# Optimization experiments

Measured on AMD Instinct MI355X. Metric: run time of the kernel, lower is better.

## Reference

```python
import jax, jax.numpy as jnp
import numpy as np

N, L, I, H, D = 8192, 8, 256, 512, 8
PER = N // D  # nodes per depth level; level 0 nodes are tree roots


def setup_inputs() -> dict:
    key = jax.random.key(0)
    ks = jax.random.split(key, 9)
    s = 0.05
    x_seq = jax.random.normal(ks[0], (N, L, I), jnp.float32)
    # GRU params (torch nn.GRU layout, gate order r,z,n), stored transposed [in, 3H]
    W_ih = jax.random.normal(ks[1], (I, 3 * H), jnp.float32) * s
    W_hh = jax.random.normal(ks[2], (H, 3 * H), jnp.float32) * s
    b_ih = jax.random.normal(ks[3], (3 * H,), jnp.float32) * s
    b_hh = jax.random.normal(ks[4], (3 * H,), jnp.float32) * s
    # Child-sum TreeLSTM params: x-projections for i,o,u,f and recurrent U's
    Wx = jax.random.normal(ks[5], (H, 4 * H), jnp.float32) * s
    bx = jax.random.normal(ks[6], (4 * H,), jnp.float32) * s
    U_iou = jax.random.normal(ks[7], (H, 3 * H), jnp.float32) * s
    U_f = jax.random.normal(ks[8], (H, H), jnp.float32) * s
    # Forest structure: D levels of PER nodes; node at level d>0 has a random
    # parent at level d-1; roots (level 0) point at themselves (contribution is
    # zero because their own state is still zero when level 0 is processed).
    rng = np.random.default_rng(0)
    depth = np.repeat(np.arange(D), PER).astype(np.int32)
    parent = np.arange(N, dtype=np.int32)
    for d in range(1, D):
        parent[d * PER:(d + 1) * PER] = rng.integers((d - 1) * PER, d * PER, PER)
    root_ids = np.arange(PER, dtype=np.int32)
    return {
        "x_seq": x_seq, "W_ih": W_ih, "W_hh": W_hh, "b_ih": b_ih, "b_hh": b_hh,
        "Wx": Wx, "bx": bx, "U_iou": U_iou, "U_f": U_f,
        "parent": jnp.asarray(parent), "depth": jnp.asarray(depth),
        "root_ids": jnp.asarray(root_ids), "n_levels": D,
    }


def reference(x_seq, W_ih, W_hh, b_ih, b_hh, Wx, bx, U_iou, U_f,
              parent, depth, root_ids, n_levels):
    n = x_seq.shape[0]
    h_dim = W_hh.shape[0]

    # --- GRU over each node's encoding sequence (all nodes batched) ---
    def gru_step(h, x_t):  # h: [N,H], x_t: [N,I]
        gi = x_t @ W_ih + b_ih
        gh = h @ W_hh + b_hh
        ir, iz, inn = jnp.split(gi, 3, axis=-1)
        hr, hz, hn = jnp.split(gh, 3, axis=-1)
        r = jax.nn.sigmoid(ir + hr)
        z = jax.nn.sigmoid(iz + hz)
        ng = jnp.tanh(inn + r * hn)
        return (1.0 - z) * ng + z * h, None

    h0 = jnp.zeros((n, h_dim), x_seq.dtype)
    enc, _ = jax.lax.scan(gru_step, h0, jnp.swapaxes(x_seq, 0, 1))  # [N,H]

    # --- Child-sum TreeLSTM, processed leaves -> roots by depth level ---
    xg = enc @ Wx + bx  # [N,4H]
    xi, xo, xu, xf = jnp.split(xg, 4, axis=-1)
    c = jnp.zeros((n, h_dim), x_seq.dtype)
    h = jnp.zeros((n, h_dim), x_seq.dtype)
    for level in range(n_levels - 1, -1, -1):
        h_sum = jax.ops.segment_sum(h, parent, num_segments=n)  # sum over children
        giou = h_sum @ U_iou
        i = jax.nn.sigmoid(xi + giou[:, :h_dim])
        o = jax.nn.sigmoid(xo + giou[:, h_dim:2 * h_dim])
        u = jnp.tanh(xu + giou[:, 2 * h_dim:])
        # per-child forget gate uses parent's x projection and child's h
        f = jax.nn.sigmoid(xf[parent] + h @ U_f)
        fc = jax.ops.segment_sum(f * c, parent, num_segments=n)
        c_new = i * u + fc
        mask = (depth == level)[:, None]
        c = jnp.where(mask, c_new, c)
        h = jnp.where(mask, o * jnp.tanh(c_new), h)

    # root states per tree, stacked as [2, n_trees, H] -> (c_root, h_root)
    return jnp.stack([c[root_ids], h[root_ids]])
```

## Files before the change

kernel.cpp:

```cpp
#include <hip/hip_runtime.h>
#include <math.h>

typedef short bf16x8 __attribute__((ext_vector_type(8)));
typedef float f32x4 __attribute__((ext_vector_type(4)));

__device__ __forceinline__ float sigf(float x) {
    return __builtin_amdgcn_rcpf(1.f + __expf(-x));
}
__device__ __forceinline__ float tanhf_fast(float x) {
    const float e = __expf(2.f * x);
    return 1.f - 2.f * __builtin_amdgcn_rcpf(e + 1.f);
}

__device__ __forceinline__ unsigned short f2bf(float f) {
    union { float f; unsigned u; } v; v.f = f;
    unsigned r = (v.u + 0x7FFFu + ((v.u >> 16) & 1u)) >> 16;
    return (unsigned short)r;
}
__device__ __forceinline__ float bf2f(unsigned short u) {
    union { unsigned u; float f; } v; v.u = ((unsigned)u) << 16; return v.f;
}

__device__ __forceinline__ void gload16(const unsigned short* g, unsigned short* l) {
    __builtin_amdgcn_global_load_lds(
        (const __attribute__((address_space(1))) void*)g,
        (__attribute__((address_space(3))) void*)l, 16, 0, 0);
}

__device__ __forceinline__ int swz(int slot, int row) {
    return (slot ^ ((row >> 1) & 3)) * 8;
}
__device__ __forceinline__ int tix(int ml, int jl) {
    return ((ml >> 4) * 2 + (jl >> 5)) * 512 + (ml & 15) * 32 + (jl & 31);
}

__global__ void cvt_f32_bf16(const float* __restrict__ src,
                             unsigned short* __restrict__ dst, int n)
{
    const int i = (blockIdx.x * blockDim.x + threadIdx.x) * 4;
    if (i >= n) return;
    const float4 v = *reinterpret_cast<const float4*>(src + i);
    ushort4 o;
    o.x = f2bf(v.x); o.y = f2bf(v.y); o.z = f2bf(v.z); o.w = f2bf(v.w);
    *reinterpret_cast<ushort4*>(dst + i) = o;
}

__global__ void transpose_cvt(const float* __restrict__ src,
                              unsigned short* __restrict__ dst,
                              int rows, int cols)
{
    __shared__ float tile[32][33];
    const int bc = blockIdx.x * 32, br = blockIdx.y * 32;
    const int tx = threadIdx.x, ty = threadIdx.y;
    #pragma unroll
    for (int i = 0; i < 32; i += 8)
        tile[ty + i][tx] = src[(size_t)(br + ty + i) * cols + bc + tx];
    __syncthreads();
    #pragma unroll
    for (int i = 0; i < 32; i += 8)
        dst[(size_t)(bc + ty + i) * rows + br + tx] = f2bf(tile[tx][ty + i]);
}

__global__ __launch_bounds__(256)
void gemm_bf16out(const unsigned short* __restrict__ A,
                  const unsigned short* __restrict__ BT,
                  const float* __restrict__ bias,
                  unsigned short* __restrict__ Cb, int M, int N, int K,
                  int ncols)
{
    const int nwg = (int)gridDim.x;
    const int l = ((int)blockIdx.x & 7) * (nwg >> 3) + ((int)blockIdx.x >> 3);
    const int m0 = (l / ncols) * 128, n0 = (l % ncols) * 128;
    const int tid = (int)threadIdx.x, lane = tid & 63, wid = tid >> 6;
    const int wm = wid >> 1, wn = wid & 1;
    const int fr = lane & 15, kg = lane >> 4;
    const int lrow = lane >> 2;
    const int scol = swz(lane & 3, lrow);

    __shared__ unsigned short smem[3 * 8192];

    f32x4 acc[4][4];
    #pragma unroll
    for (int i = 0; i < 4; ++i)
        #pragma unroll
        for (int j = 0; j < 4; ++j)
            acc[i][j] = (f32x4){0.f, 0.f, 0.f, 0.f};

    auto stage = [&](int buf, int kt) {
        const int k0 = kt * 32;
        unsigned short* base = &smem[buf * 8192];
        #pragma unroll
        for (int q = 0; q < 4; ++q) {
            const int c = wid * 4 + q;
            const unsigned short* g = (c < 8)
                ? A + (size_t)(m0 + c * 16 + lrow) * K + k0 + scol
                : BT + (size_t)(n0 + (c - 8) * 16 + lrow) * K + k0 + scol;
            gload16(g, base + c * 512);
        }
    };

    const int nkt = K >> 5;
    stage(0, 0); stage(1, 1); stage(2, 2);
    int cur = 0;

    for (int kt = 0; kt < nkt; ++kt) {
        if (kt + 2 < nkt)      asm volatile("s_waitcnt vmcnt(8)" ::: "memory");
        else if (kt + 1 < nkt) asm volatile("s_waitcnt vmcnt(4)" ::: "memory");
        else                   asm volatile("s_waitcnt vmcnt(0)" ::: "memory");
        __builtin_amdgcn_s_barrier();

        const unsigned short* sb = &smem[cur * 8192];
        bf16x8 af[4], bf[4];
        #pragma unroll
        for (int mi = 0; mi < 4; ++mi) {
            const int row = wm * 64 + mi * 16 + fr;
            af[mi] = *reinterpret_cast<const bf16x8*>(&sb[row * 32 + swz(kg, row)]);
        }
        #pragma unroll
        for (int ni = 0; ni < 4; ++ni) {
            const int row = wn * 64 + ni * 16 + fr;
            bf[ni] = *reinterpret_cast<const bf16x8*>(&sb[4096 + row * 32 + swz(kg, row)]);
        }
        asm volatile("s_waitcnt lgkmcnt(0)" ::: "memory");
        __builtin_amdgcn_s_barrier();
        if (kt + 3 < nkt) stage(cur, kt + 3);

        __builtin_amdgcn_s_setprio(1);
        #pragma unroll
        for (int mi = 0; mi < 4; ++mi)
            #pragma unroll
            for (int ni = 0; ni < 4; ++ni)
                acc[mi][ni] = __builtin_amdgcn_mfma_f32_16x16x32_bf16(
                    af[mi], bf[ni], acc[mi][ni], 0, 0, 0);
        __builtin_amdgcn_s_setprio(0);
        cur = (cur == 2) ? 0 : cur + 1;
    }

    #pragma unroll
    for (int ni = 0; ni < 4; ++ni) {
        const int nl = wn * 64 + ni * 16 + fr;
        const float bv = bias[n0 + nl];
        #pragma unroll
        for (int mi = 0; mi < 4; ++mi)
            #pragma unroll
            for (int r = 0; r < 4; ++r) {
                const int ml = wm * 64 + mi * 16 + kg * 4 + r;
                smem[ml * 132 + nl] = f2bf(acc[mi][ni][r] + bv);
            }
    }
    __syncthreads();
    #pragma unroll
    for (int e = 0; e < 8; ++e) {
        const int id = tid + e * 256;
        const int row = id >> 4, cw = id & 15;
        const int4 v = *reinterpret_cast<const int4*>(&smem[row * 132 + cw * 8]);
        *reinterpret_cast<int4*>(&Cb[(size_t)(m0 + row) * N + n0 + cw * 8]) = v;
    }
}

__global__ void gru_step0(const unsigned short* __restrict__ gi,
                          unsigned short* __restrict__ hbo,
                          const float* __restrict__ b_hh)
{
    constexpr int H = 512, G3H = 1536, L = 8;
    const int idx = blockIdx.x * blockDim.x + threadIdx.x;
    const int m = idx >> 6, jv = idx & 63;
    const size_t gb = (size_t)m * L * G3H + jv * 8;
    const bf16x8 gr8 = *reinterpret_cast<const bf16x8*>(gi + gb);
    const bf16x8 gz8 = *reinterpret_cast<const bf16x8*>(gi + gb + H);
    const bf16x8 gn8 = *reinterpret_cast<const bf16x8*>(gi + gb + 2 * H);
    bf16x8 o;
    #pragma unroll
    for (int k = 0; k < 8; ++k) {
        const int j = jv * 8 + k;
        const float r = sigf(bf2f((unsigned short)gr8[k]) + b_hh[j]);
        const float z = sigf(bf2f((unsigned short)gz8[k]) + b_hh[H + j]);
        const float n = tanhf_fast(bf2f((unsigned short)gn8[k]) + r * b_hh[2 * H + j]);
        o[k] = (short)f2bf((1.f - z) * n);
    }
    *reinterpret_cast<bf16x8*>(hbo + (size_t)m * H + jv * 8) = o;
}

__global__ __launch_bounds__(256, 4)
void gru_step(const unsigned short* __restrict__ gi,
              int t,
              const unsigned short* __restrict__ hbi,
              unsigned short* __restrict__ hbo,
              const unsigned short* __restrict__ WhhT,
              const float* __restrict__ b_hh)
{
    constexpr int H = 512, G3H = 1536, L = 8;
    const int m0 = blockIdx.x * 64, j0 = blockIdx.y * 64;
    const int tid = (int)threadIdx.x, lane = tid & 63, wid = tid >> 6;
    const int wm = wid >> 1, wn = wid & 1;
    const int fr = lane & 15, kg = lane >> 4;
    const int lrow = lane >> 2;
    const int scol = swz(lane & 3, lrow);
    const int ucol = (lane & 3) * 8;

    __shared__ unsigned short smem[2 * 8192];

    f32x4 ar[2][2], az[2][2], ah[2][2];
    #pragma unroll
    for (int i = 0; i < 2; ++i)
        #pragma unroll
        for (int j = 0; j < 2; ++j) {
            ar[i][j] = (f32x4){0.f, 0.f, 0.f, 0.f};
            az[i][j] = (f32x4){0.f, 0.f, 0.f, 0.f};
            ah[i][j] = (f32x4){0.f, 0.f, 0.f, 0.f};
        }

    constexpr int nkt = H / 32;

    auto stage = [&](int buf, int kt) {
        const int k0 = kt * 32;
        unsigned short* base = &smem[buf * 8192];
        #pragma unroll
        for (int q = 0; q < 4; ++q) {
            const int c = wid * 4 + q;
            if (c < 4) {
                const unsigned short* g =
                    hbi + (size_t)(m0 + c * 16 + lrow) * H + k0 + scol;
                gload16(g, base + c * 512);
            } else {
                const int gate = (c - 4) >> 2, rowg = (c - 4) & 3;
                const unsigned short* g =
                    WhhT + (size_t)(gate * H + j0 + rowg * 16 + lrow) * H + k0 + scol;
                gload16(g, base + c * 512);
            }
        }
    };

    stage(0, 0); stage(1, 1);

    for (int kt = 0; kt < nkt; ++kt) {
        if (kt + 1 < nkt) asm volatile("s_waitcnt vmcnt(4)" ::: "memory");
        else              asm volatile("s_waitcnt vmcnt(0)" ::: "memory");
        __builtin_amdgcn_s_barrier();

        const unsigned short* sb = &smem[(kt & 1) * 8192];
        bf16x8 af[2], bfr[2], bfz[2], bfn[2];
        #pragma unroll
        for (int mi = 0; mi < 2; ++mi) {
            const int row = wm * 32 + mi * 16 + fr;
            af[mi] = *reinterpret_cast<const bf16x8*>(&sb[row * 32 + swz(kg, row)]);
        }
        #pragma unroll
        for (int ni = 0; ni < 2; ++ni) {
            const int row = wn * 32 + ni * 16 + fr;
            const int sw = swz(kg, row);
            bfr[ni] = *reinterpret_cast<const bf16x8*>(&sb[2048 + (row) * 32 + sw]);
            bfz[ni] = *reinterpret_cast<const bf16x8*>(&sb[2048 + (64 + row) * 32 + sw]);
            bfn[ni] = *reinterpret_cast<const bf16x8*>(&sb[2048 + (128 + row) * 32 + sw]);
        }
        asm volatile("s_waitcnt lgkmcnt(0)" ::: "memory");
        __builtin_amdgcn_s_barrier();
        if (kt + 2 < nkt) stage(kt & 1, kt + 2);

        __builtin_amdgcn_s_setprio(1);
        #pragma unroll
        for (int mi = 0; mi < 2; ++mi)
            #pragma unroll
            for (int ni = 0; ni < 2; ++ni) {
                ar[mi][ni] = __builtin_amdgcn_mfma_f32_16x16x32_bf16(af[mi], bfr[ni], ar[mi][ni], 0, 0, 0);
                az[mi][ni] = __builtin_amdgcn_mfma_f32_16x16x32_bf16(af[mi], bfz[ni], az[mi][ni], 0, 0, 0);
                ah[mi][ni] = __builtin_amdgcn_mfma_f32_16x16x32_bf16(af[mi], bfn[ni], ah[mi][ni], 0, 0, 0);
            }
        __builtin_amdgcn_s_setprio(0);
    }

    #pragma unroll
    for (int q = 0; q < 8; ++q) {
        const int c = wid * 8 + q;
        if (c < 24) {
            const int g = c >> 3, cc = c & 7;
            const int rowg = cc >> 1, colg = cc & 1;
            const unsigned short* src = gi
                + ((size_t)(m0 + rowg * 16 + lrow) * L + t) * G3H
                + g * H + j0 + colg * 32 + ucol;
            gload16(src, &smem[g * 4096 + cc * 512]);
        } else {
            const int cc = c - 24;
            const int rowg = cc >> 1, colg = cc & 1;
            const unsigned short* src = hbi
                + (size_t)(m0 + rowg * 16 + lrow) * H + j0 + colg * 32 + ucol;
            gload16(src, &smem[12288 + cc * 512]);
        }
    }
    __syncthreads();

    unsigned short res[2][2][4];
    #pragma unroll
    for (int ni = 0; ni < 2; ++ni) {
        const int jl = wn * 32 + ni * 16 + fr;
        const int j = j0 + jl;
        const float bhr = b_hh[j], bhz = b_hh[H + j], bhn = b_hh[2 * H + j];
        #pragma unroll
        for (int mi = 0; mi < 2; ++mi) {
            #pragma unroll
            for (int r = 0; r < 4; ++r) {
                const int ml = wm * 32 + mi * 16 + kg * 4 + r;
                const int ix = tix(ml, jl);
                const float gr = bf2f(smem[ix]);
                const float gz = bf2f(smem[4096 + ix]);
                const float gn = bf2f(smem[8192 + ix]);
                const float hv = bf2f(smem[12288 + ix]);
                const float rg = sigf(ar[mi][ni][r] + gr + bhr);
                const float zg = sigf(az[mi][ni][r] + gz + bhz);
                const float ng = tanhf_fast(gn + rg * (ah[mi][ni][r] + bhn));
                res[ni][mi][r] = f2bf((1.f - zg) * ng + zg * hv);
            }
        }
    }
    __syncthreads();

    #pragma unroll
    for (int ni = 0; ni < 2; ++ni) {
        const int jl = wn * 32 + ni * 16 + fr;
        #pragma unroll
        for (int mi = 0; mi < 2; ++mi)
            #pragma unroll
            for (int r = 0; r < 4; ++r) {
                const int ml = wm * 32 + mi * 16 + kg * 4 + r;
                smem[tix(ml, jl)] = res[ni][mi][r];
            }
    }
    __syncthreads();

    #pragma unroll
    for (int e = 0; e < 2; ++e) {
        const int id = tid + e * 256;
        const int ml = id >> 3, jw = id & 7;
        const int4 v = *reinterpret_cast<const int4*>(
            &smem[((ml >> 4) * 2 + (jw >> 2)) * 512 + (ml & 15) * 32 + (jw & 3) * 8]);
        *reinterpret_cast<int4*>(&hbo[(size_t)(m0 + ml) * H + j0 + jw * 8]) = v;
    }
}

__global__ __launch_bounds__(256, 4)
void tree_gemm(const unsigned short* __restrict__ hTb,
               const unsigned short* __restrict__ UcombT,
               const unsigned short* __restrict__ xgb,
               const float* __restrict__ cT,
               const int* __restrict__ parent,
               int cstart, int pstart,
               float* __restrict__ giou,
               float* __restrict__ fcs)
{
    constexpr int H = 512, N4H = 2048, G3H = 1536;
    const int nwg = (int)gridDim.x;
    const int l = ((int)blockIdx.x & 7) * (nwg >> 3) + ((int)blockIdx.x >> 3);
    const int m0 = (l >> 5) * 64, n0 = (l & 31) * 64;
    const int tid = (int)threadIdx.x, lane = tid & 63, wid = tid >> 6;
    const int wm = wid >> 1, wn = wid & 1;
    const int fr = lane & 15, kg = lane >> 4;
    const int lrow = lane >> 2;
    const int scol = swz(lane & 3, lrow);

    __shared__ unsigned short smem[3 * 4096];

    f32x4 acc[2][2];
    #pragma unroll
    for (int i = 0; i < 2; ++i)
        #pragma unroll
        for (int j = 0; j < 2; ++j)
            acc[i][j] = (f32x4){0.f, 0.f, 0.f, 0.f};

    auto stage = [&](int buf, int kt) {
        const int k0 = kt * 32;
        unsigned short* base = &smem[buf * 4096];
        #pragma unroll
        for (int q = 0; q < 2; ++q) {
            const int c = wid * 2 + q;
            const unsigned short* g = (c < 4)
                ? hTb + (size_t)(cstart + m0 + c * 16 + lrow) * H + k0 + scol
                : UcombT + (size_t)(n0 + (c - 4) * 16 + lrow) * H + k0 + scol;
            gload16(g, base + c * 512);
        }
    };

    constexpr int nkt = H / 32;
    stage(0, 0); stage(1, 1); stage(2, 2);
    int cur = 0;

    for (int kt = 0; kt < nkt; ++kt) {
        if (kt + 2 < nkt)      asm volatile("s_waitcnt vmcnt(4)" ::: "memory");
        else if (kt + 1 < nkt) asm volatile("s_waitcnt vmcnt(2)" ::: "memory");
        else                   asm volatile("s_waitcnt vmcnt(0)" ::: "memory");
        __builtin_amdgcn_s_barrier();

        const unsigned short* sb = &smem[cur * 4096];
        bf16x8 af[2], bf[2];
        #pragma unroll
        for (int mi = 0; mi < 2; ++mi) {
            const int row = wm * 32 + mi * 16 + fr;
            af[mi] = *reinterpret_cast<const bf16x8*>(&sb[row * 32 + swz(kg, row)]);
        }
        #pragma unroll
        for (int ni = 0; ni < 2; ++ni) {
            const int row = wn * 32 + ni * 16 + fr;
            bf[ni] = *reinterpret_cast<const bf16x8*>(&sb[2048 + row * 32 + swz(kg, row)]);
        }
        asm volatile("s_waitcnt lgkmcnt(0)" ::: "memory");
        __builtin_amdgcn_s_barrier();
        if (kt + 3 < nkt) stage(cur, kt + 3);

        __builtin_amdgcn_s_setprio(1);
        #pragma unroll
        for (int mi = 0; mi < 2; ++mi)
            #pragma unroll
            for (int ni = 0; ni < 2; ++ni)
                acc[mi][ni] = __builtin_amdgcn_mfma_f32_16x16x32_bf16(
                    af[mi], bf[ni], acc[mi][ni], 0, 0, 0);
        __builtin_amdgcn_s_setprio(0);
        cur = (cur == 2) ? 0 : cur + 1;
    }

    if (n0 < G3H) {
        #pragma unroll
        for (int mi = 0; mi < 2; ++mi)
            #pragma unroll
            for (int r = 0; r < 4; ++r) {
                const int m = m0 + wm * 32 + mi * 16 + kg * 4 + r;
                const int p = parent[cstart + m] - pstart;
                #pragma unroll
                for (int ni = 0; ni < 2; ++ni) {
                    const int n = n0 + wn * 32 + ni * 16 + fr;
                    atomicAdd(&giou[(size_t)p * G3H + n], acc[mi][ni][r]);
                }
            }
    } else {
        #pragma unroll
        for (int mi = 0; mi < 2; ++mi)
            #pragma unroll
            for (int r = 0; r < 4; ++r) {
                const int m = m0 + wm * 32 + mi * 16 + kg * 4 + r;
                const int child = cstart + m;
                const int p = parent[child];
                #pragma unroll
                for (int ni = 0; ni < 2; ++ni) {
                    const int jf = n0 + wn * 32 + ni * 16 + fr - G3H;
                    const float f = sigf(acc[mi][ni][r] +
                                         bf2f(xgb[(size_t)p * N4H + G3H + jf]));
                    atomicAdd(&fcs[(size_t)(p - pstart) * H + jf],
                              f * cT[(size_t)child * H + jf]);
                }
            }
    }
}

__global__ void level_update(const unsigned short* __restrict__ xgb,
                             float* __restrict__ giou,
                             float* __restrict__ fcs,
                             float* __restrict__ cT, float* __restrict__ hT,
                             unsigned short* __restrict__ hb, int pstart,
                             float* __restrict__ outp, int PH)
{
    constexpr int H = 512, N4H = 2048, G3H = 1536;
    const int idx = blockIdx.x * blockDim.x + threadIdx.x;
    const int pi = idx >> 9, j = idx & (H - 1);
    const int p = pstart + pi;
    const size_t xb4 = (size_t)p * N4H;
    const size_t gb = (size_t)pi * G3H;
    const float ig = sigf(bf2f(xgb[xb4 + j]) + giou[gb + j]);
    const float og = sigf(bf2f(xgb[xb4 + H + j]) + giou[gb + H + j]);
    const float ug = tanhf_fast(bf2f(xgb[xb4 + 2 * H + j]) + giou[gb + 2 * H + j]);
    const float cn = ig * ug + fcs[idx];
    const float hn = og * tanhf_fast(cn);
    if (outp) {
        outp[idx] = cn;
        outp[(size_t)PH + idx] = hn;
    } else {
        const size_t off = (size_t)p * H + j;
        cT[off] = cn;
        hT[off] = hn;
        hb[off] = f2bf(hn);
        giou[gb + j] = 0.f;
        giou[gb + H + j] = 0.f;
        giou[gb + 2 * H + j] = 0.f;
        fcs[idx] = 0.f;
    }
}

extern "C" void kernel_launch(void* const* d_in, const int* in_sizes, int n_in,
                              void* d_out, int out_size, void* d_ws, size_t ws_size,
                              hipStream_t stream)
{
    const float* x_seq = (const float*)d_in[0];
    const float* W_ih  = (const float*)d_in[1];
    const float* W_hh  = (const float*)d_in[2];
    const float* b_ih  = (const float*)d_in[3];
    const float* b_hh  = (const float*)d_in[4];
    const float* Wx    = (const float*)d_in[5];
    const float* bx    = (const float*)d_in[6];
    const float* U_iou = (const float*)d_in[7];
    const float* U_f   = (const float*)d_in[8];
    const int* parent  = (const int*)d_in[9];

    const int threeH = in_sizes[3];
    const int H   = threeH / 3;
    const int I   = in_sizes[1] / threeH;
    const int N   = in_sizes[9];
    const int L   = in_sizes[0] / (N * I);
    const int PER = in_sizes[11];
    const int D   = N / PER;

    const size_t NH = (size_t)N * H;
    const size_t PH = (size_t)PER * H;

    char* p = (char*)d_ws;
    const size_t xb_sz  = (size_t)N * L * I * 2;
    const size_t xgb_sz = (size_t)N * 4 * H * 2;
    const size_t zone_sz = xb_sz > xgb_sz ? xb_sz : xgb_sz;
    unsigned short* xb  = (unsigned short*)p;
    unsigned short* xgb = (unsigned short*)p;    p += zone_sz;
    unsigned short* gi  = (unsigned short*)p;    p += (size_t)N * L * threeH * 2;
    unsigned short* hb0 = (unsigned short*)p;    p += NH * 2;
    unsigned short* hb1 = (unsigned short*)p;    p += NH * 2;
    unsigned short* WihT = (unsigned short*)p;   p += (size_t)threeH * I * 2;
    unsigned short* WhhT = (unsigned short*)p;   p += (size_t)threeH * H * 2;
    unsigned short* WxT  = (unsigned short*)p;   p += (size_t)4 * H * H * 2;
    unsigned short* UcombT = (unsigned short*)p; p += (size_t)4 * H * H * 2;
    if ((size_t)(p - (char*)d_ws) > ws_size) return;
    float* cT   = (float*)gi;
    float* hT   = cT + NH;
    float* giou = hT + NH;
    float* fcs  = giou + PH * 3;

    {
        const int n = N * L * I;
        cvt_f32_bf16<<<(n / 4 + 255) / 256, 256, 0, stream>>>(x_seq, xb, n);
        dim3 blk(32, 8);
        transpose_cvt<<<dim3(threeH / 32, I / 32), blk, 0, stream>>>(W_ih, WihT, I, threeH);
        transpose_cvt<<<dim3(threeH / 32, H / 32), blk, 0, stream>>>(W_hh, WhhT, H, threeH);
        transpose_cvt<<<dim3(4 * H / 32, H / 32), blk, 0, stream>>>(Wx, WxT, H, 4 * H);
        transpose_cvt<<<dim3(threeH / 32, H / 32), blk, 0, stream>>>(U_iou, UcombT, H, threeH);
        transpose_cvt<<<dim3(H / 32, H / 32), blk, 0, stream>>>(
            U_f, UcombT + (size_t)threeH * H, H, H);
    }

    gemm_bf16out<<<(N * L / 128) * (threeH / 128), 256, 0, stream>>>(
        xb, WihT, b_ih, gi, N * L, threeH, I, threeH / 128);

    gru_step0<<<(int)(NH / 8 / 256), 256, 0, stream>>>(gi, hb1, b_hh);
    {
        dim3 grid(N / 64, H / 64);
        for (int t = 1; t < L; ++t) {
            const unsigned short* hin = (t & 1) ? hb1 : hb0;
            unsigned short* hout = (t & 1) ? hb0 : hb1;
            gru_step<<<grid, 256, 0, stream>>>(gi, t, hin, hout, WhhT, b_hh);
        }
    }

    gemm_bf16out<<<(N / 128) * (4 * H / 128), 256, 0, stream>>>(
        hb0, WxT, bx, xgb, N, 4 * H, H, 4 * H / 128);

    hipMemsetAsync(giou, 0, PH * 4 * 4, stream);
    unsigned short* hTb = hb1;
    const int pw_blocks = (int)(PH / 256);

    for (int lvl = D - 1; lvl >= 0; --lvl) {
        const int pstart = lvl * PER;
        const int cstart = (lvl + 1) * PER;

        if (lvl < D - 1)
            tree_gemm<<<(PER / 64) * (4 * H / 64), 256, 0, stream>>>(
                hTb, UcombT, xgb, cT, parent, cstart, pstart, giou, fcs);

        level_update<<<pw_blocks, 256, 0, stream>>>(
            xgb, giou, fcs, cT, hT, hTb, pstart,
            (lvl == 0) ? (float*)d_out : nullptr, (int)PH);
    }
}
```

Measured before the change: 475.3 us.

## Deepen GRU and TreeLSTM pipelines, prefetch GRU epilogue operands during mainloop

The GRU step kernel moves from a double to a triple-buffered K pipeline with a constant vmcnt wait. In the last iterations it issues the epilogue loads of the gi gates and the previous h into the freed buffers, so they overlap the final MFMAs instead of following the loop. The TreeLSTM GEMM kernel goes from a 3-stage to a 4-stage buffer ring. Both kernels use more LDS, and the GRU launch bound drops to 3 waves, which can reduce occupancy.

```diff
diff --git a/kernel.cpp b/kernel.cpp
--- a/kernel.cpp
+++ b/kernel.cpp
@@ -181,7 +181,7 @@
     *reinterpret_cast<bf16x8*>(hbo + (size_t)m * H + jv * 8) = o;
 }
 
-__global__ __launch_bounds__(256, 4)
+__global__ __launch_bounds__(256, 3)
 void gru_step(const unsigned short* __restrict__ gi,
               int t,
               const unsigned short* __restrict__ hbi,
@@ -198,7 +198,7 @@
     const int scol = swz(lane & 3, lrow);
     const int ucol = (lane & 3) * 8;
 
-    __shared__ unsigned short smem[2 * 8192];
+    __shared__ unsigned short smem[3 * 8192];
 
     f32x4 ar[2][2], az[2][2], ah[2][2];
     #pragma unroll
@@ -230,15 +230,35 @@
             }
         }
     };
-
-    stage(0, 0); stage(1, 1);
+    auto stage_epi = [&](int ep) {
+        unsigned short* base = &smem[(ep + 1) * 8192];
+        #pragma unroll
+        for (int q = 0; q < 4; ++q) {
+            const int c = wid * 4 + q;
+            const int part = c >> 3, cc = c & 7;
+            const int rowg = cc >> 1, colg = cc & 1;
+            const unsigned short* src;
+            if (ep == 0)
+                src = gi + ((size_t)(m0 + rowg * 16 + lrow) * L + t) * G3H
+                         + part * H + j0 + colg * 32 + ucol;
+            else if (part == 0)
+                src = gi + ((size_t)(m0 + rowg * 16 + lrow) * L + t) * G3H
+                         + 2 * H + j0 + colg * 32 + ucol;
+            else
+                src = hbi + (size_t)(m0 + rowg * 16 + lrow) * H
+                          + j0 + colg * 32 + ucol;
+            gload16(src, base + part * 4096 + cc * 512);
+        }
+    };
+
+    stage(0, 0); stage(1, 1); stage(2, 2);
+    int cur = 0;
 
     for (int kt = 0; kt < nkt; ++kt) {
-        if (kt + 1 < nkt) asm volatile("s_waitcnt vmcnt(4)" ::: "memory");
-        else              asm volatile("s_waitcnt vmcnt(0)" ::: "memory");
+        asm volatile("s_waitcnt vmcnt(8)" ::: "memory");
         __builtin_amdgcn_s_barrier();
 
-        const unsigned short* sb = &smem[(kt & 1) * 8192];
+        const unsigned short* sb = &smem[cur * 8192];
         bf16x8 af[2], bfr[2], bfz[2], bfn[2];
         #pragma unroll
         for (int mi = 0; mi < 2; ++mi) {
@@ -255,7 +275,9 @@
         }
         asm volatile("s_waitcnt lgkmcnt(0)" ::: "memory");
         __builtin_amdgcn_s_barrier();
-        if (kt + 2 < nkt) stage(kt & 1, kt + 2);
+        if (kt + 3 < nkt)       stage(cur, kt + 3);
+        else if (kt == nkt - 3) stage_epi(0);
+        else if (kt == nkt - 2) stage_epi(1);
 
         __builtin_amdgcn_s_setprio(1);
         #pragma unroll
@@ -267,27 +289,11 @@
                 ah[mi][ni] = __builtin_amdgcn_mfma_f32_16x16x32_bf16(af[mi], bfn[ni], ah[mi][ni], 0, 0, 0);
             }
         __builtin_amdgcn_s_setprio(0);
-    }
-
-    #pragma unroll
-    for (int q = 0; q < 8; ++q) {
-        const int c = wid * 8 + q;
-        if (c < 24) {
-            const int g = c >> 3, cc = c & 7;
-            const int rowg = cc >> 1, colg = cc & 1;
-            const unsigned short* src = gi
-                + ((size_t)(m0 + rowg * 16 + lrow) * L + t) * G3H
-                + g * H + j0 + colg * 32 + ucol;
-            gload16(src, &smem[g * 4096 + cc * 512]);
-        } else {
-            const int cc = c - 24;
-            const int rowg = cc >> 1, colg = cc & 1;
-            const unsigned short* src = hbi
-                + (size_t)(m0 + rowg * 16 + lrow) * H + j0 + colg * 32 + ucol;
-            gload16(src, &smem[12288 + cc * 512]);
-        }
-    }
-    __syncthreads();
+        cur = (cur == 2) ? 0 : cur + 1;
+    }
+
+    asm volatile("s_waitcnt vmcnt(0)" ::: "memory");
+    __builtin_amdgcn_s_barrier();
 
     unsigned short res[2][2][4];
     #pragma unroll
@@ -301,10 +307,10 @@
             for (int r = 0; r < 4; ++r) {
                 const int ml = wm * 32 + mi * 16 + kg * 4 + r;
                 const int ix = tix(ml, jl);
-                const float gr = bf2f(smem[ix]);
-                const float gz = bf2f(smem[4096 + ix]);
-                const float gn = bf2f(smem[8192 + ix]);
-                const float hv = bf2f(smem[12288 + ix]);
+                const float gr = bf2f(smem[8192 + ix]);
+                const float gz = bf2f(smem[12288 + ix]);
+                const float gn = bf2f(smem[16384 + ix]);
+                const float hv = bf2f(smem[20480 + ix]);
                 const float rg = sigf(ar[mi][ni][r] + gr + bhr);
                 const float zg = sigf(az[mi][ni][r] + gz + bhz);
                 const float ng = tanhf_fast(gn + rg * (ah[mi][ni][r] + bhn));
@@ -312,7 +318,6 @@
             }
         }
     }
-    __syncthreads();
 
     #pragma unroll
     for (int ni = 0; ni < 2; ++ni) {
@@ -357,7 +362,7 @@
     const int lrow = lane >> 2;
     const int scol = swz(lane & 3, lrow);
 
-    __shared__ unsigned short smem[3 * 4096];
+    __shared__ unsigned short smem[4 * 4096];
 
     f32x4 acc[2][2];
     #pragma unroll
@@ -380,11 +385,12 @@
     };
 
     constexpr int nkt = H / 32;
-    stage(0, 0); stage(1, 1); stage(2, 2);
+    stage(0, 0); stage(1, 1); stage(2, 2); stage(3, 3);
     int cur = 0;
 
     for (int kt = 0; kt < nkt; ++kt) {
-        if (kt + 2 < nkt)      asm volatile("s_waitcnt vmcnt(4)" ::: "memory");
+        if (kt + 3 < nkt)      asm volatile("s_waitcnt vmcnt(6)" ::: "memory");
+        else if (kt + 2 < nkt) asm volatile("s_waitcnt vmcnt(4)" ::: "memory");
         else if (kt + 1 < nkt) asm volatile("s_waitcnt vmcnt(2)" ::: "memory");
         else                   asm volatile("s_waitcnt vmcnt(0)" ::: "memory");
         __builtin_amdgcn_s_barrier();
@@ -403,7 +409,7 @@
         }
         asm volatile("s_waitcnt lgkmcnt(0)" ::: "memory");
         __builtin_amdgcn_s_barrier();
-        if (kt + 3 < nkt) stage(cur, kt + 3);
+        if (kt + 4 < nkt) stage(cur, kt + 4);
 
         __builtin_amdgcn_s_setprio(1);
         #pragma unroll
@@ -413,7 +419,7 @@
                 acc[mi][ni] = __builtin_amdgcn_mfma_f32_16x16x32_bf16(
                     af[mi], bf[ni], acc[mi][ni], 0, 0, 0);
         __builtin_amdgcn_s_setprio(0);
-        cur = (cur == 2) ? 0 : cur + 1;
+        cur = (cur == 3) ? 0 : cur + 1;
     }
 
     if (n0 < G3H) {
```

Result: no change. 473.0 us (-0.5%).
